# Optimization experiments

Hardware: AMD Instinct MI355X
Metric: run time of the kernel (lower is better)

Reference implementation:

```python
import jax, jax.numpy as jnp
import numpy as np

N_NODES = 20000
N_EDGES = 320000
N_GRAPHS = 256
D = 256
L = 4
EPS = 1e-5


def setup_inputs() -> dict:
    key = jax.random.key(0)
    ks = jax.random.split(key, 20)
    x = jax.random.normal(ks[0], (N_NODES, D), dtype=jnp.float32)
    edge_index = jax.random.randint(ks[1], (2, N_EDGES), 0, N_NODES, dtype=jnp.int64)
    batch = jnp.sort(jax.random.randint(ks[2], (N_NODES,), 0, N_GRAPHS, dtype=jnp.int64))
    s = 1.0 / np.sqrt(D)
    Wl = jax.random.uniform(ks[3], (L, D, D), jnp.float32, -s, s)
    bl = jax.random.uniform(ks[4], (L, D), jnp.float32, -s, s)
    Wr = jax.random.uniform(ks[5], (L, D, D), jnp.float32, -s, s)
    gamma = jnp.ones((L, D), jnp.float32)
    beta = jnp.zeros((L, D), jnp.float32)
    fc1_w = jax.random.uniform(ks[6], (D, 128), jnp.float32, -s, s)
    fc1_b = jax.random.uniform(ks[7], (128,), jnp.float32, -s, s)
    s2 = 1.0 / np.sqrt(128)
    fc2_w = jax.random.uniform(ks[8], (128, 64), jnp.float32, -s2, s2)
    fc2_b = jax.random.uniform(ks[9], (64,), jnp.float32, -s2, s2)
    s3 = 1.0 / np.sqrt(64)
    fc3_w = jax.random.uniform(ks[10], (64, 10), jnp.float32, -s3, s3)
    fc3_b = jax.random.uniform(ks[11], (10,), jnp.float32, -s3, s3)
    return dict(x=x, edge_index=edge_index, batch=batch, Wl=Wl, bl=bl, Wr=Wr,
                gamma=gamma, beta=beta, fc1_w=fc1_w, fc1_b=fc1_b,
                fc2_w=fc2_w, fc2_b=fc2_b, fc3_w=fc3_w, fc3_b=fc3_b)


def reference(x, edge_index, batch, Wl, bl, Wr, gamma, beta,
              fc1_w, fc1_b, fc2_w, fc2_b, fc3_w, fc3_b):
    src, dst = edge_index[0], edge_index[1]
    # in-degree for mean aggregation (zero-degree nodes -> 0 aggregate)
    deg = jax.ops.segment_sum(jnp.ones((src.shape[0],), x.dtype), dst, num_segments=N_NODES)
    inv_deg = jnp.where(deg > 0, 1.0 / jnp.maximum(deg, 1.0), 0.0)[:, None]
    for i in range(L):
        # SAGEConv: mean-aggregate neighbors, then lin_l(agg) + lin_r(x)
        agg = jax.ops.segment_sum(x[src], dst, num_segments=N_NODES) * inv_deg
        h = agg @ Wl[i] + bl[i] + x @ Wr[i]
        # BatchNorm (training mode: biased batch statistics over nodes)
        mu = jnp.mean(h, axis=0)
        var = jnp.mean(jnp.square(h - mu), axis=0)
        h = (h - mu) * jax.lax.rsqrt(var + EPS) * gamma[i] + beta[i]
        x = jax.nn.relu(h)
    # global_mean_pool over graphs
    cnt = jax.ops.segment_sum(jnp.ones((N_NODES,), x.dtype), batch, num_segments=N_GRAPHS)
    g = jax.ops.segment_sum(x, batch, num_segments=N_GRAPHS) / jnp.maximum(cnt, 1.0)[:, None]
    # MLP classifier: 256 -> 128 -> 64 -> 10
    g = jax.nn.relu(g @ fc1_w + fc1_b)
    g = jax.nn.relu(g @ fc2_w + fc2_b)
    return g @ fc3_w + fc3_b
```

## Files before the change

### kernel.cpp

```cpp
#include <hip/hip_runtime.h>
#include <hip/hip_bf16.h>

#define NN 20000
#define NE 320000
#define NG 256
#define DD 256
#define NL 4
#define NBX2 157

typedef __attribute__((ext_vector_type(8))) short short8;
typedef __attribute__((ext_vector_type(4))) float float4_t;

__device__ __forceinline__ int ld_idx(const int* __restrict__ p, int i, int f64) {
    return f64 ? p[2 * i] : p[i];
}

__device__ __forceinline__ float bf2f(ushort u) {
    return __uint_as_float(((unsigned)u) << 16);
}

__device__ __forceinline__ ushort f2bf(float f) {
    __hip_bfloat16 b = __float2bfloat16(f);
    return *(ushort*)&b;
}


__global__ void k_init(const int* __restrict__ ei, const int* __restrict__ batch,
                       const ushort* __restrict__ x, int* __restrict__ flags,
                       int* __restrict__ deg) {
    int gid = blockIdx.x * 256 + threadIdx.x;
    for (int i = gid; i < NN; i += gridDim.x * 256) deg[i] = 0;
    if (blockIdx.x == 0) {
        __shared__ int cnt0, cnt1, weird;
        int t = threadIdx.x;
        if (t == 0) { cnt0 = 0; cnt1 = 0; weird = 0; }
        __syncthreads();
        for (int tt = t; tt < 512; tt += 256) {
            if (ei[2 * tt + 1] != 0) atomicAdd(&cnt0, 1);
            int i = tt * 9;
            if (batch[2 * i + 1] != 0) atomicAdd(&cnt1, 1);
#pragma unroll
            for (int j = 0; j < 16; j++) {
                ushort v = x[tt * 16 + j];
                if (((v >> 7) & 0xFF) >= 0xC0) atomicAdd(&weird, 1);
            }
        }
        __syncthreads();
        if (t == 0) {
            flags[0] = (cnt0 == 0) ? 1 : 0;
            flags[1] = (cnt1 == 0) ? 1 : 0;
            flags[2] = (weird == 0) ? 1 : 0;
        }
    }
}


__global__ void k_cvt8(const void* __restrict__ in, ushort* __restrict__ outb,
                       const int* __restrict__ fl) {
    int i = blockIdx.x * 256 + threadIdx.x;
    if (fl[2]) {
        *(int4*)(outb + (size_t)i * 8) = ((const int4*)in)[i];
    } else {
        const float* f = (const float*)in + (size_t)i * 8;
        ushort ov[8];
#pragma unroll
        for (int d = 0; d < 8; d++) ov[d] = f2bf(f[d]);
        *(int4*)(outb + (size_t)i * 8) = *(int4*)ov;
    }
}

#define POFF_BL   0
#define POFF_GA   1024
#define POFF_BE   2048
#define POFF_F1W  3072
#define POFF_F1B  35840
#define POFF_F2W  35968
#define POFF_F2B  44160
#define POFF_F3W  44224
#define POFF_F3B  44864
#define PTOT      44874

__global__ void k_cvtp(const void* s0, const void* s1, const void* s2, const void* s3,
                       const void* s4, const void* s5, const void* s6, const void* s7,
                       const void* s8, ushort* __restrict__ dst, const int* __restrict__ fl) {
    int i = blockIdx.x * 256 + threadIdx.x;
    if (i >= PTOT) return;
    const int offs[10] = {POFF_BL, POFF_GA, POFF_BE, POFF_F1W, POFF_F1B,
                          POFF_F2W, POFF_F2B, POFF_F3W, POFF_F3B, PTOT};
    const void* srcs[9] = {s0, s1, s2, s3, s4, s5, s6, s7, s8};
    int seg = 0;
#pragma unroll
    for (int k = 1; k < 9; k++) if (i >= offs[k]) seg = k;
    int local = i - offs[seg];
    if (fl[2]) dst[i] = ((const ushort*)srcs[seg])[local];
    else       dst[i] = f2bf(((const float*)srcs[seg])[local]);
}


__global__ __launch_bounds__(256) void k_transT(const void* __restrict__ WL,
                                                const void* __restrict__ WR,
                                                ushort* __restrict__ wtL,
                                                ushort* __restrict__ wtR,
                                                const int* __restrict__ fl) {
    __shared__ ushort T[64][65];
    int bid = blockIdx.x;
    int lm = bid >> 4;
    int tile = bid & 15;
    int tk = (tile >> 2) * 64, tn = (tile & 3) * 64;
    const void* W = (lm >= 4) ? WR : WL;
    ushort* Wt = (lm >= 4) ? wtR : wtL;
    size_t base = (size_t)(lm & 3) << 16;
    int t = threadIdx.x;
    int f32 = !fl[2];
#pragma unroll
    for (int i = 0; i < 16; i++) {
        int flat = t + i * 256;
        int r = flat >> 6, c = flat & 63;
        size_t src = base + (size_t)(tk + r) * 256 + tn + c;
        ushort v = f32 ? f2bf(((const float*)W)[src]) : ((const ushort*)W)[src];
        T[c][r] = v;
    }
    __syncthreads();
#pragma unroll
    for (int i = 0; i < 16; i++) {
        int flat = t + i * 256;
        int r = flat >> 6, c = flat & 63;
        Wt[base + (size_t)(tn + r) * 256 + tk + c] = T[r][c];
    }
}


__global__ void k_degree(const int* __restrict__ ei, int* __restrict__ deg,
                         const int* __restrict__ fl) {
    int e = blockIdx.x * 256 + threadIdx.x;
    if (e < NE) {
        int src = ld_idx(ei, e, fl[0]);
        int dst = ld_idx(ei, NE + e, fl[0]);
        if ((unsigned)dst < NN && (unsigned)src < NN) atomicAdd(&deg[dst], 1);
    }
}

__global__ void k_scan2(const int* __restrict__ deg, int* __restrict__ rowst,
                        int* __restrict__ cursor, float* __restrict__ invdeg) {
    __shared__ int part[1024];
    int t = threadIdx.x;
    const int per = (NN + 1023) / 1024;
    int lo = t * per;
    int hi = lo + per; if (hi > NN) hi = NN;
    int s = 0;
    for (int i = lo; i < hi; i++) s += deg[i];
    part[t] = s;
    __syncthreads();
    if (t == 0) {
        int run = 0;
        for (int i = 0; i < 1024; i++) { int v = part[i]; part[i] = run; run += v; }
        rowst[NN] = run;
    }
    __syncthreads();
    int run = part[t];
    for (int i = lo; i < hi; i++) {
        int d = deg[i];
        rowst[i] = run;
        cursor[i] = run;
        invdeg[i] = d > 0 ? 1.0f / (float)d : 0.0f;
        run += d;
    }
}

__global__ void k_fill(const int* __restrict__ ei, int* __restrict__ cursor,
                       int* __restrict__ csr, const int* __restrict__ fl) {
    int e = blockIdx.x * 256 + threadIdx.x;
    if (e < NE) {
        int src = ld_idx(ei, e, fl[0]);
        int dst = ld_idx(ei, NE + e, fl[0]);
        if ((unsigned)dst < NN && (unsigned)src < NN) {
            int p = atomicAdd(&cursor[dst], 1);
            if ((unsigned)p < NE) csr[p] = src;
        }
    }
}

__global__ void k_gstart(const int* __restrict__ batch, int* __restrict__ gstart,
                         const int* __restrict__ fl) {
    int i = blockIdx.x * 256 + threadIdx.x;
    if (i >= NN) return;
    int b = ld_idx(batch, i, fl[1]);
    int bp = (i == 0) ? -1 : ld_idx(batch, i - 1, fl[1]);
    for (int g = bp + 1; g <= b; g++)
        if ((unsigned)g <= NG) gstart[g] = i;
    if (i == NN - 1)
        for (int g = b + 1; g <= NG; g++) gstart[g] = NN;
}


template <int BNF>
__global__ __launch_bounds__(256) void k_agg4(
    const ushort* __restrict__ X, const int* __restrict__ rs,
    const int* __restrict__ csr, const float* __restrict__ invdeg,
    const float* __restrict__ bnsc, const float* __restrict__ bnsh,
    ushort* __restrict__ AGG) {
    int node = blockIdx.x * 4 + (threadIdx.x >> 6);
    if (node >= NN) return;
    int h = (threadIdx.x >> 5) & 1;
    int j = threadIdx.x & 31;
    float sc[8], sh[8];
    if (BNF) {
        float4 a0 = *(const float4*)(bnsc + j * 8);
        float4 a1 = *(const float4*)(bnsc + j * 8 + 4);
        float4 b0 = *(const float4*)(bnsh + j * 8);
        float4 b1 = *(const float4*)(bnsh + j * 8 + 4);
        sc[0] = a0.x; sc[1] = a0.y; sc[2] = a0.z; sc[3] = a0.w;
        sc[4] = a1.x; sc[5] = a1.y; sc[6] = a1.z; sc[7] = a1.w;
        sh[0] = b0.x; sh[1] = b0.y; sh[2] = b0.z; sh[3] = b0.w;
        sh[4] = b1.x; sh[5] = b1.y; sh[6] = b1.z; sh[7] = b1.w;
    }
    int e0 = rs[node], e1 = rs[node + 1];
    float acc[8] = {};
    int e = e0 + h;
    for (; e + 6 < e1; e += 8) {
        int s0 = csr[e], s1 = csr[e + 2], s2 = csr[e + 4], s3 = csr[e + 6];
        int4 v0 = *(const int4*)(X + (size_t)s0 * DD + j * 8);
        int4 v1 = *(const int4*)(X + (size_t)s1 * DD + j * 8);
        int4 v2 = *(const int4*)(X + (size_t)s2 * DD + j * 8);
        int4 v3 = *(const int4*)(X + (size_t)s3 * DD + j * 8);
        const ushort* u0 = (const ushort*)&v0;
        const ushort* u1 = (const ushort*)&v1;
        const ushort* u2 = (const ushort*)&v2;
        const ushort* u3 = (const ushort*)&v3;
#pragma unroll
        for (int d = 0; d < 8; d++) {
            float r0 = bf2f(u0[d]), r1 = bf2f(u1[d]), r2 = bf2f(u2[d]), r3 = bf2f(u3[d]);
            if (BNF) {
                r0 = fmaxf(r0 * sc[d] + sh[d], 0.0f);
                r1 = fmaxf(r1 * sc[d] + sh[d], 0.0f);
                r2 = fmaxf(r2 * sc[d] + sh[d], 0.0f);
                r3 = fmaxf(r3 * sc[d] + sh[d], 0.0f);
            }
            acc[d] += (r0 + r1) + (r2 + r3);
        }
    }
    for (; e < e1; e += 2) {
        int s = csr[e];
        int4 v = *(const int4*)(X + (size_t)s * DD + j * 8);
        const ushort* u = (const ushort*)&v;
#pragma unroll
        for (int d = 0; d < 8; d++) {
            float r = bf2f(u[d]);
            if (BNF) r = fmaxf(r * sc[d] + sh[d], 0.0f);
            acc[d] += r;
        }
    }
#pragma unroll
    for (int d = 0; d < 8; d++)
        acc[d] += __shfl_down(acc[d], 32);
    if (h == 0) {
        float inv = invdeg[node];
        ushort ov[8];
#pragma unroll
        for (int d = 0; d < 8; d++) ov[d] = f2bf(acc[d] * inv);
        *(int4*)(AGG + (size_t)node * DD + j * 8) = *(int4*)ov;
    }
}


template <int BNF>
__global__ __launch_bounds__(256) void k_gemm3(
    const ushort* __restrict__ A1, const ushort* __restrict__ A2,
    const ushort* __restrict__ Wt1, const ushort* __restrict__ Wt2,
    const ushort* __restrict__ bias,
    const float* __restrict__ bnsc, const float* __restrict__ bnsh,
    ushort* __restrict__ H, float* __restrict__ psum, float* __restrict__ psq) {
    __shared__ ushort Als[128][40];
    __shared__ ushort Bls[128][40];
    __shared__ float colsum[128];
    __shared__ float colsq[128];
    const int m0 = blockIdx.x * 128;
    const int n0 = blockIdx.y * 128;
    const int tid = threadIdx.x;
    const int w = tid >> 6, l = tid & 63, lr = l & 15, q = l >> 4;
    const int wm = (w >> 1) * 64, wn = (w & 1) * 64;
    float4_t acc[4][4] = {};

    const int srow = tid >> 1;
    const int sce = (tid & 1) * 16;

    for (int mat = 0; mat < 2; ++mat) {
        const ushort* A = mat ? A2 : A1;
        const ushort* Wt = mat ? Wt2 : Wt1;
        for (int k0 = 0; k0 < 256; k0 += 32) {
            int ar = m0 + srow; if (ar >= NN) ar = NN - 1;
            int4 av0 = *(const int4*)(A + (size_t)ar * DD + k0 + sce);
            int4 av1 = *(const int4*)(A + (size_t)ar * DD + k0 + sce + 8);
            int4 bv0 = *(const int4*)(Wt + (size_t)(n0 + srow) * DD + k0 + sce);
            int4 bv1 = *(const int4*)(Wt + (size_t)(n0 + srow) * DD + k0 + sce + 8);
            if (BNF && mat == 1) {
                float scv[16], shv[16];
#pragma unroll
                for (int g = 0; g < 4; g++) {
                    float4 s4 = *(const float4*)(bnsc + k0 + sce + g * 4);
                    float4 h4 = *(const float4*)(bnsh + k0 + sce + g * 4);
                    scv[g*4] = s4.x; scv[g*4+1] = s4.y; scv[g*4+2] = s4.z; scv[g*4+3] = s4.w;
                    shv[g*4] = h4.x; shv[g*4+1] = h4.y; shv[g*4+2] = h4.z; shv[g*4+3] = h4.w;
                }
                ushort* u0 = (ushort*)&av0;
                ushort* u1 = (ushort*)&av1;
#pragma unroll
                for (int d = 0; d < 8; d++) {
                    u0[d] = f2bf(fmaxf(bf2f(u0[d]) * scv[d] + shv[d], 0.0f));
                    u1[d] = f2bf(fmaxf(bf2f(u1[d]) * scv[8 + d] + shv[8 + d], 0.0f));
                }
            }
            *(int4*)&Als[srow][sce] = av0;
            *(int4*)&Als[srow][sce + 8] = av1;
            *(int4*)&Bls[srow][sce] = bv0;
            *(int4*)&Bls[srow][sce + 8] = bv1;
            __syncthreads();
            short8 af[4], bf[4];
#pragma unroll
            for (int im = 0; im < 4; im++)
                af[im] = *(const short8*)&Als[wm + im * 16 + lr][q * 8];
#pragma unroll
            for (int in = 0; in < 4; in++)
                bf[in] = *(const short8*)&Bls[wn + in * 16 + lr][q * 8];
#pragma unroll
            for (int im = 0; im < 4; im++)
#pragma unroll
                for (int in = 0; in < 4; in++)
                    acc[im][in] = __builtin_amdgcn_mfma_f32_16x16x32_bf16(
                        af[im], bf[in], acc[im][in], 0, 0, 0);
            __syncthreads();
        }
    }
    if (tid < 128) { colsum[tid] = 0.0f; colsq[tid] = 0.0f; }
    __syncthreads();

    int mbase = m0 + wm + q * 4;
#pragma unroll
    for (int in = 0; in < 4; in++) {
        int n = n0 + wn + in * 16 + lr;
        float b = bf2f(bias[n]);
        float s = 0.0f, s2 = 0.0f;
#pragma unroll
        for (int im = 0; im < 4; im++) {
#pragma unroll
            for (int i = 0; i < 4; i++) {
                int m = mbase + im * 16 + i;
                if (m < NN) {
                    float hv = acc[im][in][i] + b;
                    ushort hb = f2bf(hv);
                    H[(size_t)m * DD + n] = hb;
                    float hq = bf2f(hb);
                    s += hq;
                    s2 += hq * hq;
                }
            }
        }
        s += __shfl_xor(s, 16);  s += __shfl_xor(s, 32);
        s2 += __shfl_xor(s2, 16); s2 += __shfl_xor(s2, 32);
        if (q == 0) {
            atomicAdd(&colsum[wn + in * 16 + lr], s);
            atomicAdd(&colsq[wn + in * 16 + lr], s2);
        }
    }
    __syncthreads();
    if (tid < 128) {
        psum[(size_t)blockIdx.x * DD + n0 + tid] = colsum[tid];
        psq[(size_t)blockIdx.x * DD + n0 + tid] = colsq[tid];
    }
}


__global__ __launch_bounds__(64) void k_bnfinal3(
    const float* __restrict__ psum, const float* __restrict__ psq,
    const ushort* __restrict__ gamma, const ushort* __restrict__ beta,
    float* __restrict__ scale, float* __restrict__ shift) {
    int c = blockIdx.x;
    int t = threadIdx.x;
    float s = 0.0f, s2 = 0.0f;
    for (int b = t; b < NBX2; b += 64) {
        s += psum[(size_t)b * DD + c];
        s2 += psq[(size_t)b * DD + c];
    }
#pragma unroll
    for (int o = 32; o; o >>= 1) {
        s += __shfl_down(s, o);
        s2 += __shfl_down(s2, o);
    }
    if (t == 0) {
        float mu = s * (1.0f / NN);
        float var = s2 * (1.0f / NN) - mu * mu;
        if (var < 0.0f) var = 0.0f;
        float rstd = rsqrtf(var + 1e-5f);
        float g = bf2f(gamma[c]);
        float b2 = bf2f(beta[c]);
        scale[c] = g * rstd;
        shift[c] = b2 - mu * g * rstd;
    }
}


__global__ void k_pool3(const ushort* __restrict__ Hb, const float* __restrict__ scale,
                        const float* __restrict__ shift, const int* __restrict__ gstart,
                        float* __restrict__ gmean) {
    int g = blockIdx.x;
    int t = threadIdx.x;
    int s0 = gstart[g], e = gstart[g + 1];
    float sc = scale[t], sh = shift[t];
    float acc = 0.0f;
    for (int i = s0; i < e; i++)
        acc += fmaxf(bf2f(Hb[(size_t)i * DD + t]) * sc + sh, 0.0f);
    gmean[(size_t)g * DD + t] = acc / fmaxf((float)(e - s0), 1.0f);
}

__global__ __launch_bounds__(128) void k_mlp(
    const float* __restrict__ gmean,
    const ushort* __restrict__ fc1w, const ushort* __restrict__ fc1b,
    const ushort* __restrict__ fc2w, const ushort* __restrict__ fc2b,
    const ushort* __restrict__ fc3w, const ushort* __restrict__ fc3b,
    void* __restrict__ out, const int* __restrict__ fl) {
    __shared__ float g[256];
    __shared__ float h1[128];
    __shared__ float h2[64];
    int gid = blockIdx.x;
    int t = threadIdx.x;
    g[t] = gmean[(size_t)gid * DD + t];
    g[t + 128] = gmean[(size_t)gid * DD + t + 128];
    __syncthreads();
    float a = bf2f(fc1b[t]);
    for (int k = 0; k < 256; k++)
        a += g[k] * bf2f(fc1w[k * 128 + t]);
    h1[t] = fmaxf(a, 0.0f);
    __syncthreads();
    if (t < 64) {
        float a2 = bf2f(fc2b[t]);
        for (int k = 0; k < 128; k++)
            a2 += h1[k] * bf2f(fc2w[k * 64 + t]);
        h2[t] = fmaxf(a2, 0.0f);
    }
    __syncthreads();
    if (t < 10) {
        float a3 = bf2f(fc3b[t]);
        for (int k = 0; k < 64; k++)
            a3 += h2[k] * bf2f(fc3w[k * 10 + t]);
        if (fl[2]) ((__hip_bfloat16*)out)[gid * 10 + t] = __float2bfloat16(a3);
        else       ((float*)out)[gid * 10 + t] = a3;
    }
}


static inline char* bump(char*& p, size_t n) {
    char* r = p;
    p += (n + 255) & ~(size_t)255;
    return r;
}

extern "C" void kernel_launch(void* const* d_in, const int* in_sizes, int n_in,
                              void* d_out, int out_size, void* d_ws, size_t ws_size,
                              hipStream_t stream) {
    const void* x_in  = d_in[0];
    const int*  ei    = (const int*)d_in[1];
    const int*  batch = (const int*)d_in[2];
    const void* Wl    = d_in[3];
    const void* bl    = d_in[4];
    const void* Wr    = d_in[5];
    const void* gamma = d_in[6];
    const void* beta  = d_in[7];

    char* p = (char*)d_ws;
    int*    flags    = (int*)bump(p, 256);
    ushort* wtL      = (ushort*)bump(p, (size_t)NL * 65536 * 2);
    ushort* wtR      = (ushort*)bump(p, (size_t)NL * 65536 * 2);
    ushort* xcan     = (ushort*)bump(p, (size_t)NN * DD * 2);
    ushort* pcan     = (ushort*)bump(p, (size_t)PTOT * 2);
    int*    deg      = (int*)bump(p, NN * 4);
    int*    rowst    = (int*)bump(p, (NN + 1) * 4);
    int*    cursor   = (int*)bump(p, NN * 4);
    float*  invdeg   = (float*)bump(p, NN * 4);
    int*    csr      = (int*)bump(p, NE * 4);
    int*    gstart   = (int*)bump(p, (NG + 1) * 4);
    ushort* agg      = (ushort*)bump(p, (size_t)NN * DD * 2);
    ushort* hb0      = (ushort*)bump(p, (size_t)NN * DD * 2);
    ushort* hb1      = (ushort*)bump(p, (size_t)NN * DD * 2);
    float*  psum     = (float*)bump(p, (size_t)NBX2 * DD * 4);
    float*  psq      = (float*)bump(p, (size_t)NBX2 * DD * 4);
    float*  scale    = (float*)bump(p, DD * 4);
    float*  shift    = (float*)bump(p, DD * 4);
    float*  gmean    = (float*)bump(p, (size_t)NG * DD * 4);

    if ((size_t)(p - (char*)d_ws) > ws_size) return;

    ushort* blc = pcan + POFF_BL;
    ushort* gac = pcan + POFF_GA;
    ushort* bec = pcan + POFF_BE;
    ushort* f1w = pcan + POFF_F1W;
    ushort* f1b = pcan + POFF_F1B;
    ushort* f2w = pcan + POFF_F2W;
    ushort* f2b = pcan + POFF_F2B;
    ushort* f3w = pcan + POFF_F3W;
    ushort* f3b = pcan + POFF_F3B;

    k_init<<<80, 256, 0, stream>>>(ei, batch, (const ushort*)x_in, flags, deg);
    k_cvt8<<<NN * DD / 8 / 256, 256, 0, stream>>>(x_in, xcan, flags);
    k_transT<<<128, 256, 0, stream>>>(Wl, Wr, wtL, wtR, flags);
    k_cvtp<<<(PTOT + 255) / 256, 256, 0, stream>>>(bl, gamma, beta,
        d_in[8], d_in[9], d_in[10], d_in[11], d_in[12], d_in[13], pcan, flags);

    k_degree<<<(NE + 255) / 256, 256, 0, stream>>>(ei, deg, flags);
    k_scan2<<<1, 1024, 0, stream>>>(deg, rowst, cursor, invdeg);
    k_fill<<<(NE + 255) / 256, 256, 0, stream>>>(ei, cursor, csr, flags);
    k_gstart<<<(NN + 255) / 256, 256, 0, stream>>>(batch, gstart, flags);

    ushort* hbuf[2] = {hb0, hb1};
    const ushort* xsrc = xcan;
    for (int l = 0; l < NL; l++) {
        ushort* hdst = hbuf[l & 1];
        if (l == 0) {
            k_agg4<0><<<(NN + 3) / 4, 256, 0, stream>>>(xsrc, rowst, csr, invdeg,
                                                        scale, shift, agg);
            k_gemm3<0><<<dim3(NBX2, 2), 256, 0, stream>>>(
                agg, xsrc, wtL, wtR, blc, scale, shift, hdst, psum, psq);
        } else {
            k_agg4<1><<<(NN + 3) / 4, 256, 0, stream>>>(xsrc, rowst, csr, invdeg,
                                                        scale, shift, agg);
            k_gemm3<1><<<dim3(NBX2, 2), 256, 0, stream>>>(
                agg, xsrc, wtL + (size_t)l * 65536, wtR + (size_t)l * 65536,
                blc + l * DD, scale, shift, hdst, psum, psq);
        }
        k_bnfinal3<<<DD, 64, 0, stream>>>(psum, psq, gac + l * DD, bec + l * DD,
                                          scale, shift);
        xsrc = hdst;
    }

    k_pool3<<<NG, 256, 0, stream>>>(xsrc, scale, shift, gstart, gmean);
    k_mlp<<<NG, 128, 0, stream>>>(gmean, f1w, f1b, f2w, f2b, f3w, f3b, d_out, flags);
}
```

Measured before the change: 429.9 us.

## Fuse prep kernels, BN finalize into GEMM, pool into MLP head; widen gather

Merges the x conversion, weight transpose, parameter conversion, degree count and graph-start kernels into one block-partitioned prep kernel. The BatchNorm finalize now runs inside the GEMM: the last block to finish, detected with an atomic counter, reduces the partial sums and writes scale and shift. Pooling and the MLP are fused into one head kernel. The degree scan uses a parallel Hillis-Steele pass, and the neighbour gather issues 8 loads per iteration instead of 4. The aim is fewer kernel launches and less serial work, at the cost of one serialized last-block reduction and more register pressure in the gather.

```diff
diff --git a/kernel.cpp b/kernel.cpp
--- a/kernel.cpp
+++ b/kernel.cpp
@@ -30,6 +30,7 @@
                        int* __restrict__ deg) {
     int gid = blockIdx.x * 256 + threadIdx.x;
     for (int i = gid; i < NN; i += gridDim.x * 256) deg[i] = 0;
+    if (gid == 0) flags[8] = 0;
     if (blockIdx.x == 0) {
         __shared__ int cnt0, cnt1, weird;
         int t = threadIdx.x;
@@ -54,20 +55,6 @@
     }
 }
 
-
-__global__ void k_cvt8(const void* __restrict__ in, ushort* __restrict__ outb,
-                       const int* __restrict__ fl) {
-    int i = blockIdx.x * 256 + threadIdx.x;
-    if (fl[2]) {
-        *(int4*)(outb + (size_t)i * 8) = ((const int4*)in)[i];
-    } else {
-        const float* f = (const float*)in + (size_t)i * 8;
-        ushort ov[8];
-#pragma unroll
-        for (int d = 0; d < 8; d++) ov[d] = f2bf(f[d]);
-        *(int4*)(outb + (size_t)i * 8) = *(int4*)ov;
-    }
-}
 
 #define POFF_BL   0
 #define POFF_GA   1024
@@ -80,67 +67,97 @@
 #define POFF_F3B  44864
 #define PTOT      44874
 
-__global__ void k_cvtp(const void* s0, const void* s1, const void* s2, const void* s3,
-                       const void* s4, const void* s5, const void* s6, const void* s7,
-                       const void* s8, ushort* __restrict__ dst, const int* __restrict__ fl) {
-    int i = blockIdx.x * 256 + threadIdx.x;
-    if (i >= PTOT) return;
-    const int offs[10] = {POFF_BL, POFF_GA, POFF_BE, POFF_F1W, POFF_F1B,
-                          POFF_F2W, POFF_F2B, POFF_F3W, POFF_F3B, PTOT};
-    const void* srcs[9] = {s0, s1, s2, s3, s4, s5, s6, s7, s8};
-    int seg = 0;
-#pragma unroll
-    for (int k = 1; k < 9; k++) if (i >= offs[k]) seg = k;
-    int local = i - offs[seg];
-    if (fl[2]) dst[i] = ((const ushort*)srcs[seg])[local];
-    else       dst[i] = f2bf(((const float*)srcs[seg])[local]);
-}
-
-
-__global__ __launch_bounds__(256) void k_transT(const void* __restrict__ WL,
-                                                const void* __restrict__ WR,
-                                                ushort* __restrict__ wtL,
-                                                ushort* __restrict__ wtR,
-                                                const int* __restrict__ fl) {
-    __shared__ ushort T[64][65];
-    int bid = blockIdx.x;
-    int lm = bid >> 4;
-    int tile = bid & 15;
-    int tk = (tile >> 2) * 64, tn = (tile & 3) * 64;
-    const void* W = (lm >= 4) ? WR : WL;
-    ushort* Wt = (lm >= 4) ? wtR : wtL;
-    size_t base = (size_t)(lm & 3) << 16;
+#define NB_CVT8   2500
+#define NB_TRANS  128
+#define NB_CVTP   176
+#define NB_DEG    1250
+#define NB_GST    79
+#define B_TRANS   (NB_CVT8)
+#define B_CVTP    (B_TRANS + NB_TRANS)
+#define B_DEG     (B_CVTP + NB_CVTP)
+#define B_GST     (B_DEG + NB_DEG)
+#define NB_PREP   (B_GST + NB_GST)
+
+__global__ __launch_bounds__(256) void k_prep(
+    const void* __restrict__ x_in, const void* __restrict__ WL,
+    const void* __restrict__ WR, const int* __restrict__ ei,
+    const int* __restrict__ batch,
+    const void* s0, const void* s1, const void* s2, const void* s3,
+    const void* s4, const void* s5, const void* s6, const void* s7, const void* s8,
+    ushort* __restrict__ xcan, ushort* __restrict__ wtL, ushort* __restrict__ wtR,
+    ushort* __restrict__ pcan, int* __restrict__ deg, int* __restrict__ gstart,
+    const int* __restrict__ fl) {
+    int blk = blockIdx.x;
     int t = threadIdx.x;
-    int f32 = !fl[2];
-#pragma unroll
-    for (int i = 0; i < 16; i++) {
-        int flat = t + i * 256;
-        int r = flat >> 6, c = flat & 63;
-        size_t src = base + (size_t)(tk + r) * 256 + tn + c;
-        ushort v = f32 ? f2bf(((const float*)W)[src]) : ((const ushort*)W)[src];
-        T[c][r] = v;
-    }
-    __syncthreads();
-#pragma unroll
-    for (int i = 0; i < 16; i++) {
-        int flat = t + i * 256;
-        int r = flat >> 6, c = flat & 63;
-        Wt[base + (size_t)(tn + r) * 256 + tk + c] = T[r][c];
-    }
-}
-
-
-__global__ void k_degree(const int* __restrict__ ei, int* __restrict__ deg,
-                         const int* __restrict__ fl) {
-    int e = blockIdx.x * 256 + threadIdx.x;
-    if (e < NE) {
-        int src = ld_idx(ei, e, fl[0]);
-        int dst = ld_idx(ei, NE + e, fl[0]);
-        if ((unsigned)dst < NN && (unsigned)src < NN) atomicAdd(&deg[dst], 1);
-    }
-}
-
-__global__ void k_scan2(const int* __restrict__ deg, int* __restrict__ rowst,
+    if (blk < B_TRANS) {
+        int i = blk * 256 + t;
+        if (fl[2]) {
+            *(int4*)(xcan + (size_t)i * 8) = ((const int4*)x_in)[i];
+        } else {
+            const float* f = (const float*)x_in + (size_t)i * 8;
+            ushort ov[8];
+#pragma unroll
+            for (int d = 0; d < 8; d++) ov[d] = f2bf(f[d]);
+            *(int4*)(xcan + (size_t)i * 8) = *(int4*)ov;
+        }
+    } else if (blk < B_CVTP) {
+        __shared__ ushort T[64][65];
+        int bid = blk - B_TRANS;
+        int lm = bid >> 4;
+        int tile = bid & 15;
+        int tk = (tile >> 2) * 64, tn = (tile & 3) * 64;
+        const void* W = (lm >= 4) ? WR : WL;
+        ushort* Wt = (lm >= 4) ? wtR : wtL;
+        size_t base = (size_t)(lm & 3) << 16;
+        int f32 = !fl[2];
+#pragma unroll
+        for (int i = 0; i < 16; i++) {
+            int flat = t + i * 256;
+            int r = flat >> 6, c = flat & 63;
+            size_t src = base + (size_t)(tk + r) * 256 + tn + c;
+            ushort v = f32 ? f2bf(((const float*)W)[src]) : ((const ushort*)W)[src];
+            T[c][r] = v;
+        }
+        __syncthreads();
+#pragma unroll
+        for (int i = 0; i < 16; i++) {
+            int flat = t + i * 256;
+            int r = flat >> 6, c = flat & 63;
+            Wt[base + (size_t)(tn + r) * 256 + tk + c] = T[r][c];
+        }
+    } else if (blk < B_DEG) {
+        int i = (blk - B_CVTP) * 256 + t;
+        if (i >= PTOT) return;
+        const int offs[10] = {POFF_BL, POFF_GA, POFF_BE, POFF_F1W, POFF_F1B,
+                              POFF_F2W, POFF_F2B, POFF_F3W, POFF_F3B, PTOT};
+        const void* srcs[9] = {s0, s1, s2, s3, s4, s5, s6, s7, s8};
+        int seg = 0;
+#pragma unroll
+        for (int k = 1; k < 9; k++) if (i >= offs[k]) seg = k;
+        int local = i - offs[seg];
+        if (fl[2]) pcan[i] = ((const ushort*)srcs[seg])[local];
+        else       pcan[i] = f2bf(((const float*)srcs[seg])[local]);
+    } else if (blk < B_GST) {
+        int e = (blk - B_DEG) * 256 + t;
+        if (e < NE) {
+            int src = ld_idx(ei, e, fl[0]);
+            int dst = ld_idx(ei, NE + e, fl[0]);
+            if ((unsigned)dst < NN && (unsigned)src < NN) atomicAdd(&deg[dst], 1);
+        }
+    } else {
+        int i = (blk - B_GST) * 256 + t;
+        if (i >= NN) return;
+        int b = ld_idx(batch, i, fl[1]);
+        int bp = (i == 0) ? -1 : ld_idx(batch, i - 1, fl[1]);
+        for (int g = bp + 1; g <= b; g++)
+            if ((unsigned)g <= NG) gstart[g] = i;
+        if (i == NN - 1)
+            for (int g = b + 1; g <= NG; g++) gstart[g] = NN;
+    }
+}
+
+
+__global__ void k_scan3(const int* __restrict__ deg, int* __restrict__ rowst,
                         int* __restrict__ cursor, float* __restrict__ invdeg) {
     __shared__ int part[1024];
     int t = threadIdx.x;
@@ -151,13 +168,14 @@
     for (int i = lo; i < hi; i++) s += deg[i];
     part[t] = s;
     __syncthreads();
-    if (t == 0) {
-        int run = 0;
-        for (int i = 0; i < 1024; i++) { int v = part[i]; part[i] = run; run += v; }
-        rowst[NN] = run;
-    }
-    __syncthreads();
-    int run = part[t];
+    for (int off = 1; off < 1024; off <<= 1) {
+        int v = (t >= off) ? part[t - off] : 0;
+        __syncthreads();
+        part[t] += v;
+        __syncthreads();
+    }
+    if (t == 1023) rowst[NN] = part[1023];
+    int run = part[t] - s;
     for (int i = lo; i < hi; i++) {
         int d = deg[i];
         rowst[i] = run;
@@ -178,18 +196,6 @@
             if ((unsigned)p < NE) csr[p] = src;
         }
     }
-}
-
-__global__ void k_gstart(const int* __restrict__ batch, int* __restrict__ gstart,
-                         const int* __restrict__ fl) {
-    int i = blockIdx.x * 256 + threadIdx.x;
-    if (i >= NN) return;
-    int b = ld_idx(batch, i, fl[1]);
-    int bp = (i == 0) ? -1 : ld_idx(batch, i - 1, fl[1]);
-    for (int g = bp + 1; g <= b; g++)
-        if ((unsigned)g <= NG) gstart[g] = i;
-    if (i == NN - 1)
-        for (int g = b + 1; g <= NG; g++) gstart[g] = NN;
 }
 
 
@@ -217,26 +223,38 @@
     int e0 = rs[node], e1 = rs[node + 1];
     float acc[8] = {};
     int e = e0 + h;
-    for (; e + 6 < e1; e += 8) {
-        int s0 = csr[e], s1 = csr[e + 2], s2 = csr[e + 4], s3 = csr[e + 6];
-        int4 v0 = *(const int4*)(X + (size_t)s0 * DD + j * 8);
-        int4 v1 = *(const int4*)(X + (size_t)s1 * DD + j * 8);
-        int4 v2 = *(const int4*)(X + (size_t)s2 * DD + j * 8);
-        int4 v3 = *(const int4*)(X + (size_t)s3 * DD + j * 8);
-        const ushort* u0 = (const ushort*)&v0;
-        const ushort* u1 = (const ushort*)&v1;
-        const ushort* u2 = (const ushort*)&v2;
-        const ushort* u3 = (const ushort*)&v3;
+    for (; e + 14 < e1; e += 16) {
+        int4 v[8];
+#pragma unroll
+        for (int r = 0; r < 8; r++) {
+            int s = csr[e + 2 * r];
+            v[r] = *(const int4*)(X + (size_t)s * DD + j * 8);
+        }
+#pragma unroll
+        for (int r = 0; r < 8; r++) {
+            const ushort* u = (const ushort*)&v[r];
+#pragma unroll
+            for (int d = 0; d < 8; d++) {
+                float x = bf2f(u[d]);
+                if (BNF) x = fmaxf(x * sc[d] + sh[d], 0.0f);
+                acc[d] += x;
+            }
+        }
+    }
+    for (; e + 2 < e1; e += 4) {
+        int sA = csr[e], sB = csr[e + 2];
+        int4 vA = *(const int4*)(X + (size_t)sA * DD + j * 8);
+        int4 vB = *(const int4*)(X + (size_t)sB * DD + j * 8);
+        const ushort* uA = (const ushort*)&vA;
+        const ushort* uB = (const ushort*)&vB;
 #pragma unroll
         for (int d = 0; d < 8; d++) {
-            float r0 = bf2f(u0[d]), r1 = bf2f(u1[d]), r2 = bf2f(u2[d]), r3 = bf2f(u3[d]);
+            float xA = bf2f(uA[d]), xB = bf2f(uB[d]);
             if (BNF) {
-                r0 = fmaxf(r0 * sc[d] + sh[d], 0.0f);
-                r1 = fmaxf(r1 * sc[d] + sh[d], 0.0f);
-                r2 = fmaxf(r2 * sc[d] + sh[d], 0.0f);
-                r3 = fmaxf(r3 * sc[d] + sh[d], 0.0f);
+                xA = fmaxf(xA * sc[d] + sh[d], 0.0f);
+                xB = fmaxf(xB * sc[d] + sh[d], 0.0f);
             }
-            acc[d] += (r0 + r1) + (r2 + r3);
+            acc[d] += xA + xB;
         }
     }
     for (; e < e1; e += 2) {
@@ -245,9 +263,9 @@
         const ushort* u = (const ushort*)&v;
 #pragma unroll
         for (int d = 0; d < 8; d++) {
-            float r = bf2f(u[d]);
-            if (BNF) r = fmaxf(r * sc[d] + sh[d], 0.0f);
-            acc[d] += r;
+            float x = bf2f(u[d]);
+            if (BNF) x = fmaxf(x * sc[d] + sh[d], 0.0f);
+            acc[d] += x;
         }
     }
 #pragma unroll
@@ -264,16 +282,20 @@
 
 
 template <int BNF>
-__global__ __launch_bounds__(256) void k_gemm3(
+__global__ __launch_bounds__(256) void k_gemm4(
     const ushort* __restrict__ A1, const ushort* __restrict__ A2,
     const ushort* __restrict__ Wt1, const ushort* __restrict__ Wt2,
     const ushort* __restrict__ bias,
     const float* __restrict__ bnsc, const float* __restrict__ bnsh,
-    ushort* __restrict__ H, float* __restrict__ psum, float* __restrict__ psq) {
+    const ushort* __restrict__ gamma, const ushort* __restrict__ beta,
+    ushort* __restrict__ H, float* __restrict__ psum, float* __restrict__ psq,
+    float* __restrict__ oscale, float* __restrict__ oshift,
+    int* __restrict__ donecnt) {
     __shared__ ushort Als[128][40];
     __shared__ ushort Bls[128][40];
     __shared__ float colsum[128];
     __shared__ float colsq[128];
+    __shared__ int lastflag;
     const int m0 = blockIdx.x * 128;
     const int n0 = blockIdx.y * 128;
     const int tid = threadIdx.x;
@@ -367,53 +389,38 @@
         psum[(size_t)blockIdx.x * DD + n0 + tid] = colsum[tid];
         psq[(size_t)blockIdx.x * DD + n0 + tid] = colsq[tid];
     }
-}
-
-
-__global__ __launch_bounds__(64) void k_bnfinal3(
-    const float* __restrict__ psum, const float* __restrict__ psq,
-    const ushort* __restrict__ gamma, const ushort* __restrict__ beta,
-    float* __restrict__ scale, float* __restrict__ shift) {
-    int c = blockIdx.x;
-    int t = threadIdx.x;
+    __threadfence();
+    if (tid == 0) {
+        int v = atomicAdd(donecnt, 1);
+        lastflag = (v == NBX2 * 2 - 1);
+    }
+    __syncthreads();
+    if (!lastflag) return;
+    __threadfence();
+    const volatile float* vs = psum;
+    const volatile float* vq = psq;
+    int c = tid;
     float s = 0.0f, s2 = 0.0f;
-    for (int b = t; b < NBX2; b += 64) {
-        s += psum[(size_t)b * DD + c];
-        s2 += psq[(size_t)b * DD + c];
-    }
-#pragma unroll
-    for (int o = 32; o; o >>= 1) {
-        s += __shfl_down(s, o);
-        s2 += __shfl_down(s2, o);
-    }
-    if (t == 0) {
-        float mu = s * (1.0f / NN);
-        float var = s2 * (1.0f / NN) - mu * mu;
-        if (var < 0.0f) var = 0.0f;
-        float rstd = rsqrtf(var + 1e-5f);
-        float g = bf2f(gamma[c]);
-        float b2 = bf2f(beta[c]);
-        scale[c] = g * rstd;
-        shift[c] = b2 - mu * g * rstd;
-    }
-}
-
-
-__global__ void k_pool3(const ushort* __restrict__ Hb, const float* __restrict__ scale,
-                        const float* __restrict__ shift, const int* __restrict__ gstart,
-                        float* __restrict__ gmean) {
-    int g = blockIdx.x;
-    int t = threadIdx.x;
-    int s0 = gstart[g], e = gstart[g + 1];
-    float sc = scale[t], sh = shift[t];
-    float acc = 0.0f;
-    for (int i = s0; i < e; i++)
-        acc += fmaxf(bf2f(Hb[(size_t)i * DD + t]) * sc + sh, 0.0f);
-    gmean[(size_t)g * DD + t] = acc / fmaxf((float)(e - s0), 1.0f);
-}
-
-__global__ __launch_bounds__(128) void k_mlp(
-    const float* __restrict__ gmean,
+    for (int b = 0; b < NBX2; b++) {
+        s += vs[(size_t)b * DD + c];
+        s2 += vq[(size_t)b * DD + c];
+    }
+    float mu = s * (1.0f / NN);
+    float var = s2 * (1.0f / NN) - mu * mu;
+    if (var < 0.0f) var = 0.0f;
+    float rstd = rsqrtf(var + 1e-5f);
+    float g = bf2f(gamma[c]);
+    float b2 = bf2f(beta[c]);
+    oscale[c] = g * rstd;
+    oshift[c] = b2 - mu * g * rstd;
+    __syncthreads();
+    if (tid == 0) *donecnt = 0;
+}
+
+
+__global__ __launch_bounds__(256) void k_head(
+    const ushort* __restrict__ Hb, const float* __restrict__ scale,
+    const float* __restrict__ shift, const int* __restrict__ gstart,
     const ushort* __restrict__ fc1w, const ushort* __restrict__ fc1b,
     const ushort* __restrict__ fc2w, const ushort* __restrict__ fc2b,
     const ushort* __restrict__ fc3w, const ushort* __restrict__ fc3b,
@@ -423,13 +430,19 @@
     __shared__ float h2[64];
     int gid = blockIdx.x;
     int t = threadIdx.x;
-    g[t] = gmean[(size_t)gid * DD + t];
-    g[t + 128] = gmean[(size_t)gid * DD + t + 128];
-    __syncthreads();
-    float a = bf2f(fc1b[t]);
-    for (int k = 0; k < 256; k++)
-        a += g[k] * bf2f(fc1w[k * 128 + t]);
-    h1[t] = fmaxf(a, 0.0f);
+    int s0 = gstart[gid], e = gstart[gid + 1];
+    float sc = scale[t], sh = shift[t];
+    float acc = 0.0f;
+    for (int i = s0; i < e; i++)
+        acc += fmaxf(bf2f(Hb[(size_t)i * DD + t]) * sc + sh, 0.0f);
+    g[t] = acc / fmaxf((float)(e - s0), 1.0f);
+    __syncthreads();
+    if (t < 128) {
+        float a = bf2f(fc1b[t]);
+        for (int k = 0; k < 256; k++)
+            a += g[k] * bf2f(fc1w[k * 128 + t]);
+        h1[t] = fmaxf(a, 0.0f);
+    }
     __syncthreads();
     if (t < 64) {
         float a2 = bf2f(fc2b[t]);
@@ -485,7 +498,6 @@
     float*  psq      = (float*)bump(p, (size_t)NBX2 * DD * 4);
     float*  scale    = (float*)bump(p, DD * 4);
     float*  shift    = (float*)bump(p, DD * 4);
-    float*  gmean    = (float*)bump(p, (size_t)NG * DD * 4);
 
     if ((size_t)(p - (char*)d_ws) > ws_size) return;
 
@@ -498,17 +510,15 @@
     ushort* f2b = pcan + POFF_F2B;
     ushort* f3w = pcan + POFF_F3W;
     ushort* f3b = pcan + POFF_F3B;
+    int* donecnt = flags + 8;
 
     k_init<<<80, 256, 0, stream>>>(ei, batch, (const ushort*)x_in, flags, deg);
-    k_cvt8<<<NN * DD / 8 / 256, 256, 0, stream>>>(x_in, xcan, flags);
-    k_transT<<<128, 256, 0, stream>>>(Wl, Wr, wtL, wtR, flags);
-    k_cvtp<<<(PTOT + 255) / 256, 256, 0, stream>>>(bl, gamma, beta,
-        d_in[8], d_in[9], d_in[10], d_in[11], d_in[12], d_in[13], pcan, flags);
-
-    k_degree<<<(NE + 255) / 256, 256, 0, stream>>>(ei, deg, flags);
-    k_scan2<<<1, 1024, 0, stream>>>(deg, rowst, cursor, invdeg);
+    k_prep<<<NB_PREP, 256, 0, stream>>>(
+        x_in, Wl, Wr, ei, batch,
+        bl, gamma, beta, d_in[8], d_in[9], d_in[10], d_in[11], d_in[12], d_in[13],
+        xcan, wtL, wtR, pcan, deg, gstart, flags);
+    k_scan3<<<1, 1024, 0, stream>>>(deg, rowst, cursor, invdeg);
     k_fill<<<(NE + 255) / 256, 256, 0, stream>>>(ei, cursor, csr, flags);
-    k_gstart<<<(NN + 255) / 256, 256, 0, stream>>>(batch, gstart, flags);
 
     ushort* hbuf[2] = {hb0, hb1};
     const ushort* xsrc = xcan;
@@ -517,20 +527,20 @@
         if (l == 0) {
             k_agg4<0><<<(NN + 3) / 4, 256, 0, stream>>>(xsrc, rowst, csr, invdeg,
                                                         scale, shift, agg);
-            k_gemm3<0><<<dim3(NBX2, 2), 256, 0, stream>>>(
-                agg, xsrc, wtL, wtR, blc, scale, shift, hdst, psum, psq);
+            k_gemm4<0><<<dim3(NBX2, 2), 256, 0, stream>>>(
+                agg, xsrc, wtL, wtR, blc, scale, shift,
+                gac, bec, hdst, psum, psq, scale, shift, donecnt);
         } else {
             k_agg4<1><<<(NN + 3) / 4, 256, 0, stream>>>(xsrc, rowst, csr, invdeg,
                                                         scale, shift, agg);
-            k_gemm3<1><<<dim3(NBX2, 2), 256, 0, stream>>>(
+            k_gemm4<1><<<dim3(NBX2, 2), 256, 0, stream>>>(
                 agg, xsrc, wtL + (size_t)l * 65536, wtR + (size_t)l * 65536,
-                blc + l * DD, scale, shift, hdst, psum, psq);
-        }
-        k_bnfinal3<<<DD, 64, 0, stream>>>(psum, psq, gac + l * DD, bec + l * DD,
-                                          scale, shift);
+                blc + l * DD, scale, shift,
+                gac + l * DD, bec + l * DD, hdst, psum, psq, scale, shift, donecnt);
+        }
         xsrc = hdst;
     }
 
-    k_pool3<<<NG, 256, 0, stream>>>(xsrc, scale, shift, gstart, gmean);
-    k_mlp<<<NG, 128, 0, stream>>>(gmean, f1w, f1b, f2w, f2b, f3w, f3b, d_out, flags);
-}
+    k_head<<<NG, 256, 0, stream>>>(xsrc, scale, shift, gstart,
+                                   f1w, f1b, f2w, f2b, f3w, f3b, d_out, flags);
+}
```

Measured after the change: 846.2 us. +96.9%, slower.
